# Kernel optimization log

Hardware: AMD Instinct MI355X
Metric: run time of the kernel (lower is better)

## Reference

```python
import jax, jax.numpy as jnp
import numpy as np

BATCH, N_MACS_PREV, CMS_PREV, NEUR_PREV = 256, 512, 8, 16
FILTER_LEN = 256
NUM_CMS, NUM_NEURONS = 32, 32
NUM_INPUTS = FILTER_LEN * CMS_PREV * NEUR_PREV  # 32768


def setup_inputs() -> dict:
    key = jax.random.key(0)
    k1, k2, k3 = jax.random.split(key, 3)
    x = jax.random.uniform(k1, (BATCH, N_MACS_PREV, CMS_PREV, NEUR_PREV), dtype=jnp.float32)
    input_filter = jax.random.randint(k2, (FILTER_LEN,), 0, N_MACS_PREV)
    # binary {0,1} weights, matching torch.randint(0, 2, ..., dtype=float32)
    weights = jax.random.randint(k3, (NUM_CMS, NUM_INPUTS, NUM_NEURONS), 0, 2).astype(jnp.float32)
    return {"x": x, "input_filter": input_filter, "weights": weights}


def reference(x, input_filter, weights):
    B = x.shape[0]
    # gather receptive field MACs and flatten: (B, num_inputs)
    xg = jnp.take(x, input_filter, axis=1).reshape(B, -1)
    # sum-normalize, nan_to_num handles all-zero rows (0/0 -> 0)
    xn = jnp.nan_to_num(xg / jnp.sum(xg, axis=-1, keepdims=True))
    # batched matmul: (B,I) x (C,I,N) -> (B,C,N)  (torch does (C,B,N) then permutes)
    acts = jnp.einsum('bi,cin->bcn', xn, weights)
    # familiarity-based softmax temperature
    familiarities = jnp.max(acts, axis=-1)          # (B, C)
    avg_fam = jnp.mean(familiarities)               # scalar
    softmax_temp = 1.0 / (avg_fam + 1e-4) - 1.0
    logits = acts / softmax_temp
    # categorical sample per (batch, cm); fixed key for determinism
    samples = jax.random.categorical(jax.random.key(42), logits, axis=-1)  # (B, C)
    # scatter one-hot write-out, int output as in torch
    out = jax.nn.one_hot(samples, NUM_NEURONS, dtype=jnp.int32)  # (B, C, N)
    return out
```

## Files before the change

kernel.cpp:

```cpp
#include <hip/hip_runtime.h>
#include <stdint.h>

#define BATCH 256
#define NMAC  512
#define ROWF  128
#define I_    32768
#define C_    32
#define N_    32
#define XROW  (NMAC * ROWF)
#define NCH   64

typedef float  f32x4  __attribute__((ext_vector_type(4)));
typedef __bf16 bf16x8 __attribute__((ext_vector_type(8)));

__device__ __forceinline__ uint32_t f2bf_rne(float f) {
    uint32_t u = __builtin_bit_cast(uint32_t, f);
    return (u + 0x7FFFu + ((u >> 16) & 1u)) >> 16;
}

__global__ __launch_bounds__(256) void k_sum(const float* __restrict__ x,
                                             const int* __restrict__ filt,
                                             float* __restrict__ S) {
    const int b = blockIdx.x;
    const int t = threadIdx.x;
    const float* xb = x + (size_t)b * XROW;
    float s = 0.f;
    for (int it = 0; it < 32; ++it) {
        int idx4 = it * 256 + t;
        int f = idx4 >> 5;
        int j4 = idx4 & 31;
        float4 v = *(const float4*)(xb + (size_t)filt[f] * ROWF + j4 * 4);
        s += v.x + v.y + v.z + v.w;
    }
    for (int o = 32; o > 0; o >>= 1) s += __shfl_down(s, o, 64);
    __shared__ float red[4];
    if ((t & 63) == 0) red[t >> 6] = s;
    __syncthreads();
    if (t == 0) S[b] = red[0] + red[1] + red[2] + red[3];
}

__global__ __launch_bounds__(256, 2) void k_gemm(const float* __restrict__ x,
                                                 const int* __restrict__ filt,
                                                 const float* __restrict__ w,
                                                 float* __restrict__ part,
                                                 float* __restrict__ raw,
                                                 int use_part) {
    __shared__ __align__(16) unsigned short afr[32 * 512];
    __shared__ __align__(16) unsigned short wfr[8 * 512];

    const int t  = threadIdx.x;
    const int l  = t & 63;
    const int wv = t >> 6;
    const int chunk = blockIdx.x & 63;
    const int c0 = (blockIdx.x >> 6) * 4;

    f32x4 acc[4][8];
#pragma unroll
    for (int bt = 0; bt < 4; ++bt)
#pragma unroll
        for (int ct = 0; ct < 8; ++ct) acc[bt][ct] = f32x4{0.f, 0.f, 0.f, 0.f};

    const int ar     = t >> 3;
    const int ai     = t & 7;
    const int a_quad = ai >> 1;
    const int a_j    = (ai & 1) * 4;
    const int wn = t & 31;
    const int wc = t >> 5;

    for (int st = 0; st < 16; ++st) {
        const int ifull = chunk * 512 + st * 32;
        const int fidx  = filt[ifull >> 7];
        const int ioff  = ifull & 127;
        const float* xs = x + (size_t)fidx * ROWF + ioff;

#pragma unroll
        for (int rr = 0; rr < 8; ++rr) {
            int row = rr * 32 + ar;
            float4 v = *(const float4*)(xs + (size_t)row * XROW + ai * 4);
            uint32_t u0 = __builtin_bit_cast(uint32_t, v.x);
            uint32_t u1 = __builtin_bit_cast(uint32_t, v.y);
            uint32_t u2 = __builtin_bit_cast(uint32_t, v.z);
            uint32_t u3 = __builtin_bit_cast(uint32_t, v.w);
            float l0 = v.x - __builtin_bit_cast(float, u0 & 0xFFFF0000u);
            float l1 = v.y - __builtin_bit_cast(float, u1 & 0xFFFF0000u);
            float l2 = v.z - __builtin_bit_cast(float, u2 & 0xFFFF0000u);
            float l3 = v.w - __builtin_bit_cast(float, u3 & 0xFFFF0000u);
            uint2 hp, lp;
            hp.x = (u0 >> 16) | (u1 & 0xFFFF0000u);
            hp.y = (u2 >> 16) | (u3 & 0xFFFF0000u);
            lp.x = f2bf_rne(l0) | (f2bf_rne(l1) << 16);
            lp.y = f2bf_rne(l2) | (f2bf_rne(l3) << 16);
            int rt   = row >> 4;
            int lane = a_quad * 16 + (row & 15);
            int base = (rt * 2) * 512 + lane * 8 + a_j;
            *(uint2*)&afr[base]       = hp;
            *(uint2*)&afr[base + 512] = lp;
        }

#pragma unroll
        for (int q = 0; q < 8; ++q) {
            int sl  = wc + 8 * q;
            int c   = sl >> 4;
            int il  = (sl & 15) * 2;
            const float* wp = w + ((size_t)(c0 + c) * I_ + ifull + il) * N_ + wn;
            uint32_t u0 = __builtin_bit_cast(uint32_t, wp[0]);
            uint32_t u1 = __builtin_bit_cast(uint32_t, wp[N_]);
            uint32_t pk = (u0 >> 16) | (u1 & 0xFFFF0000u);
            int lane = (il >> 3) * 16 + (wn & 15);
            int ct   = c * 2 + (wn >> 4);
            *(uint32_t*)&wfr[ct * 512 + lane * 8 + (il & 7)] = pk;
        }
        __syncthreads();

        bf16x8 av[4][2];
#pragma unroll
        for (int bt = 0; bt < 4; ++bt)
#pragma unroll
            for (int p = 0; p < 2; ++p)
                av[bt][p] = *(const bf16x8*)&afr[((wv * 4 + bt) * 2 + p) * 512 + l * 8];
        bf16x8 bv[8];
#pragma unroll
        for (int ct = 0; ct < 8; ++ct)
            bv[ct] = *(const bf16x8*)&wfr[ct * 512 + l * 8];
#pragma unroll
        for (int bt = 0; bt < 4; ++bt)
#pragma unroll
            for (int ct = 0; ct < 8; ++ct) {
                acc[bt][ct] = __builtin_amdgcn_mfma_f32_16x16x32_bf16(av[bt][0], bv[ct], acc[bt][ct], 0, 0, 0);
                acc[bt][ct] = __builtin_amdgcn_mfma_f32_16x16x32_bf16(av[bt][1], bv[ct], acc[bt][ct], 0, 0, 0);
            }
        __syncthreads();
    }

    const int quad = l >> 4, n15 = l & 15;
    if (use_part) {
        float* dst = part + (size_t)chunk * (BATCH * C_ * N_);
#pragma unroll
        for (int bt = 0; bt < 4; ++bt) {
#pragma unroll
            for (int ct = 0; ct < 8; ++ct) {
                int c = c0 + (ct >> 1);
                int n = (ct & 1) * 16 + n15;
#pragma unroll
                for (int r = 0; r < 4; ++r) {
                    int b = (wv * 4 + bt) * 16 + quad * 4 + r;
                    dst[((size_t)b * C_ + c) * N_ + n] = acc[bt][ct][r];
                }
            }
        }
    } else {
#pragma unroll
        for (int bt = 0; bt < 4; ++bt) {
#pragma unroll
            for (int ct = 0; ct < 8; ++ct) {
                int c = c0 + (ct >> 1);
                int n = (ct & 1) * 16 + n15;
#pragma unroll
                for (int r = 0; r < 4; ++r) {
                    int b = (wv * 4 + bt) * 16 + quad * 4 + r;
                    atomicAdd(&raw[((size_t)b * C_ + c) * N_ + n], acc[bt][ct][r]);
                }
            }
        }
    }
}

__global__ __launch_bounds__(256) void k_reduce(const float* __restrict__ part,
                                                const float* __restrict__ S,
                                                float* __restrict__ raw,
                                                float* __restrict__ fam) {
    const int i4 = blockIdx.x * 256 + threadIdx.x;
    const f32x4* p = (const f32x4*)part;
    f32x4 s = f32x4{0.f, 0.f, 0.f, 0.f};
#pragma unroll 8
    for (int ch = 0; ch < NCH; ++ch) s += p[(size_t)ch * 65536 + i4];
    ((f32x4*)raw)[i4] = s;
    float m = fmaxf(fmaxf(s[0], s[1]), fmaxf(s[2], s[3]));
    m = fmaxf(m, __shfl_xor(m, 1, 64));
    m = fmaxf(m, __shfl_xor(m, 2, 64));
    m = fmaxf(m, __shfl_xor(m, 4, 64));
    int r = i4 >> 3;
    float v = ((i4 & 7) == 0) ? (m / S[r >> 5]) : 0.f;
    for (int o = 32; o > 0; o >>= 1) v += __shfl_down(v, o, 64);
    __shared__ float red[4];
    if ((threadIdx.x & 63) == 0) red[threadIdx.x >> 6] = v;
    __syncthreads();
    if (threadIdx.x == 0) atomicAdd(fam, red[0] + red[1] + red[2] + red[3]);
}

__global__ __launch_bounds__(256) void k_fam(const float* __restrict__ raw,
                                             const float* __restrict__ S,
                                             float* __restrict__ fam) {
    int r = blockIdx.x * 256 + threadIdx.x;
    const float4* ap = (const float4*)(raw + (size_t)r * N_);
    float m = -3.0e38f;
#pragma unroll
    for (int q = 0; q < 8; ++q) {
        float4 v = ap[q];
        m = fmaxf(m, fmaxf(fmaxf(v.x, v.y), fmaxf(v.z, v.w)));
    }
    m = m / S[r >> 5];
    for (int o = 32; o > 0; o >>= 1) m += __shfl_down(m, o, 64);
    __shared__ float red[4];
    if ((threadIdx.x & 63) == 0) red[threadIdx.x >> 6] = m;
    __syncthreads();
    if (threadIdx.x == 0) atomicAdd(fam, red[0] + red[1] + red[2] + red[3]);
}

__device__ __forceinline__ uint32_t rotl32(uint32_t x, uint32_t r) {
    return (x << r) | (x >> (32u - r));
}
__device__ __forceinline__ void threefry(uint32_t k0, uint32_t k1,
                                         uint32_t x0, uint32_t x1,
                                         uint32_t& o0, uint32_t& o1) {
    uint32_t ks2 = k0 ^ k1 ^ 0x1BD11BDAu;
    x0 += k0; x1 += k1;
    x0 += x1; x1 = rotl32(x1, 13); x1 ^= x0;
    x0 += x1; x1 = rotl32(x1, 15); x1 ^= x0;
    x0 += x1; x1 = rotl32(x1, 26); x1 ^= x0;
    x0 += x1; x1 = rotl32(x1, 6);  x1 ^= x0;
    x0 += k1; x1 += ks2 + 1u;
    x0 += x1; x1 = rotl32(x1, 17); x1 ^= x0;
    x0 += x1; x1 = rotl32(x1, 29); x1 ^= x0;
    x0 += x1; x1 = rotl32(x1, 16); x1 ^= x0;
    x0 += x1; x1 = rotl32(x1, 24); x1 ^= x0;
    x0 += ks2; x1 += k0 + 2u;
    x0 += x1; x1 = rotl32(x1, 13); x1 ^= x0;
    x0 += x1; x1 = rotl32(x1, 15); x1 ^= x0;
    x0 += x1; x1 = rotl32(x1, 26); x1 ^= x0;
    x0 += x1; x1 = rotl32(x1, 6);  x1 ^= x0;
    x0 += k0; x1 += k1 + 3u;
    x0 += x1; x1 = rotl32(x1, 17); x1 ^= x0;
    x0 += x1; x1 = rotl32(x1, 29); x1 ^= x0;
    x0 += x1; x1 = rotl32(x1, 16); x1 ^= x0;
    x0 += x1; x1 = rotl32(x1, 24); x1 ^= x0;
    x0 += k1; x1 += ks2 + 4u;
    x0 += x1; x1 = rotl32(x1, 13); x1 ^= x0;
    x0 += x1; x1 = rotl32(x1, 15); x1 ^= x0;
    x0 += x1; x1 = rotl32(x1, 26); x1 ^= x0;
    x0 += x1; x1 = rotl32(x1, 6);  x1 ^= x0;
    x0 += ks2; x1 += k0 + 5u;
    o0 = x0; o1 = x1;
}

__device__ __forceinline__ float gumbel_of(uint32_t bits) {
    uint32_t fb = (bits >> 9) | 0x3F800000u;
    float f = __builtin_bit_cast(float, fb) - 1.0f;
    float u = f + 1.17549435e-38f;
    return -logf(-logf(u));
}

__global__ __launch_bounds__(256) void k_sample(const float* __restrict__ raw,
                                                const float* __restrict__ S,
                                                const float* __restrict__ fam,
                                                int* __restrict__ out) {
    int r0 = blockIdx.x * 256 + threadIdx.x;
    int r1 = r0 + 4096;
    float avg  = fam[0] * (1.0f / 8192.0f);
    float temp = 1.0f / (avg + 1e-4f) - 1.0f;
    float sA = S[r0 >> 5], sB = S[r1 >> 5];
    const float* apA = raw + (size_t)r0 * N_;
    const float* apB = raw + (size_t)r1 * N_;

    float bestA = -3.4e38f, bestB = -3.4e38f;
    int biA = 0, biB = 0;
    for (int n = 0; n < 32; ++n) {
        uint32_t iA = (uint32_t)(r0 * 32 + n);
        uint32_t iB = (uint32_t)(r1 * 32 + n);
        uint32_t a0, a1, b0, b1;
        threefry(0u, 42u, 0u, iA, a0, a1);
        threefry(0u, 42u, 0u, iB, b0, b1);
        float vA = (apA[n] / sA) / temp + gumbel_of(a0 ^ a1);
        float vB = (apB[n] / sB) / temp + gumbel_of(b0 ^ b1);
        if (vA > bestA) { bestA = vA; biA = n; }
        if (vB > bestB) { bestB = vB; biB = n; }
    }
    int4* opA = (int4*)(out + (size_t)r0 * N_);
    int4* opB = (int4*)(out + (size_t)r1 * N_);
#pragma unroll
    for (int q = 0; q < 8; ++q) {
        int4 a, b;
        a.x = (q * 4 + 0) == biA; a.y = (q * 4 + 1) == biA;
        a.z = (q * 4 + 2) == biA; a.w = (q * 4 + 3) == biA;
        b.x = (q * 4 + 0) == biB; b.y = (q * 4 + 1) == biB;
        b.z = (q * 4 + 2) == biB; b.w = (q * 4 + 3) == biB;
        opA[q] = a; opB[q] = b;
    }
}

extern "C" void kernel_launch(void* const* d_in, const int* in_sizes, int n_in,
                              void* d_out, int out_size, void* d_ws, size_t ws_size,
                              hipStream_t stream) {
    const float* x    = (const float*)d_in[0];
    const int*   filt = (const int*)d_in[1];
    const float* w    = (const float*)d_in[2];
    int* out = (int*)d_out;

    char* ws = (char*)d_ws;
    float* raw  = (float*)ws;
    float* fam  = (float*)(ws + (1 << 20));
    float* S    = (float*)(ws + (1 << 20) + 128);
    float* part = (float*)(ws + (2u << 20));

    const size_t need = (2u << 20) + (size_t)NCH * (BATCH * C_ * N_) * sizeof(float);
    const int use_part = (ws_size >= need) ? 1 : 0;

    if (use_part) {
        hipMemsetAsync(ws + (1 << 20), 0, 128, stream);
        hipLaunchKernelGGL(k_sum,    dim3(256), dim3(256), 0, stream, x, filt, S);
        hipLaunchKernelGGL(k_gemm,   dim3(512), dim3(256), 0, stream, x, filt, w, part, raw, 1);
        hipLaunchKernelGGL(k_reduce, dim3(256), dim3(256), 0, stream, part, S, raw, fam);
        hipLaunchKernelGGL(k_sample, dim3(16),  dim3(256), 0, stream, raw, S, fam, out);
    } else {
        hipMemsetAsync(ws, 0, (1 << 20) + 128, stream);
        hipLaunchKernelGGL(k_sum,    dim3(256), dim3(256), 0, stream, x, filt, S);
        hipLaunchKernelGGL(k_gemm,   dim3(512), dim3(256), 0, stream, x, filt, w, part, raw, 0);
        hipLaunchKernelGGL(k_fam,    dim3(32),  dim3(256), 0, stream, raw, S, fam);
        hipLaunchKernelGGL(k_sample, dim3(16),  dim3(256), 0, stream, raw, S, fam, out);
    }
}
```

Measured before the change: 280.7 us.

## Pre-split activations into bf16 fragments and double-buffer GEMM loads via LDS DMA

Adds a prep kernel that gathers the filtered activations once, splits them into hi/lo bf16 pairs and writes them in MFMA fragment layout to workspace. The new GEMM kernel double-buffers A tiles with global_load_lds DMA and prefetches weights into registers for the next stage, overlapping loads with MFMA work. This removes the per-block repeated gather and conversion of x across the 8 c-groups, but it adds a 32 MB intermediate write and read and needs a larger workspace. The old path is kept as a fallback.

```diff
diff --git a/kernel.cpp b/kernel.cpp
--- a/kernel.cpp
+++ b/kernel.cpp
@@ -9,6 +9,7 @@
 #define N_    32
 #define XROW  (NMAC * ROWF)
 #define NCH   64
+#define NST   16
 
 typedef float  f32x4  __attribute__((ext_vector_type(4)));
 typedef __bf16 bf16x8 __attribute__((ext_vector_type(8)));
@@ -16,6 +17,12 @@
 __device__ __forceinline__ uint32_t f2bf_rne(float f) {
     uint32_t u = __builtin_bit_cast(uint32_t, f);
     return (u + 0x7FFFu + ((u >> 16) & 1u)) >> 16;
+}
+
+__device__ __forceinline__ void gll16(const void* g, void* l) {
+    __builtin_amdgcn_global_load_lds(
+        (const __attribute__((address_space(1))) uint32_t*)g,
+        (__attribute__((address_space(3))) uint32_t*)l, 16, 0, 0);
 }
 
 __global__ __launch_bounds__(256) void k_sum(const float* __restrict__ x,
@@ -39,12 +46,150 @@
     if (t == 0) S[b] = red[0] + red[1] + red[2] + red[3];
 }
 
-__global__ __launch_bounds__(256, 2) void k_gemm(const float* __restrict__ x,
-                                                 const int* __restrict__ filt,
-                                                 const float* __restrict__ w,
-                                                 float* __restrict__ part,
-                                                 float* __restrict__ raw,
-                                                 int use_part) {
+__global__ __launch_bounds__(256) void k_prep(const float* __restrict__ x,
+                                              const int* __restrict__ filt,
+                                              unsigned short* __restrict__ prepA) {
+    const int b     = threadIdx.x;
+    const int chunk = blockIdx.x >> 4;
+    const int st    = blockIdx.x & 15;
+    const int ifull = chunk * 512 + st * 32;
+    const int fidx  = filt[ifull >> 7];
+    const int ioff  = ifull & 127;
+    const float* src = x + (size_t)b * XROW + (size_t)fidx * ROWF + ioff;
+    unsigned short* dstb = prepA + (size_t)blockIdx.x * 16384
+                         + (b >> 4) * 1024 + (b & 15) * 8;
+    float4 v[8];
+#pragma unroll
+    for (int j = 0; j < 8; ++j) v[j] = ((const float4*)src)[j];
+#pragma unroll
+    for (int kq = 0; kq < 4; ++kq) {
+        float f[8];
+        float4 a = v[kq * 2], c = v[kq * 2 + 1];
+        f[0] = a.x; f[1] = a.y; f[2] = a.z; f[3] = a.w;
+        f[4] = c.x; f[5] = c.y; f[6] = c.z; f[7] = c.w;
+        uint32_t h[4], lo[4];
+#pragma unroll
+        for (int e = 0; e < 4; ++e) {
+            uint32_t u0 = __builtin_bit_cast(uint32_t, f[2 * e]);
+            uint32_t u1 = __builtin_bit_cast(uint32_t, f[2 * e + 1]);
+            float r0 = f[2 * e]     - __builtin_bit_cast(float, u0 & 0xFFFF0000u);
+            float r1 = f[2 * e + 1] - __builtin_bit_cast(float, u1 & 0xFFFF0000u);
+            h[e]  = (u0 >> 16) | (u1 & 0xFFFF0000u);
+            lo[e] = f2bf_rne(r0) | (f2bf_rne(r1) << 16);
+        }
+        *(uint4*)&dstb[kq * 128]       = make_uint4(h[0], h[1], h[2], h[3]);
+        *(uint4*)&dstb[512 + kq * 128] = make_uint4(lo[0], lo[1], lo[2], lo[3]);
+    }
+}
+
+__global__ __launch_bounds__(256, 2) void k_gemm2(const unsigned short* __restrict__ prepA,
+                                                  const float* __restrict__ w,
+                                                  float* __restrict__ part) {
+    __shared__ __align__(16) unsigned short bufA[2][16384];
+    __shared__ __align__(16) unsigned short bufW[2][4096];
+
+    const int t  = threadIdx.x;
+    const int l  = t & 63;
+    const int wv = t >> 6;
+    const int chunk = blockIdx.x & 63;
+    const int c0 = (blockIdx.x >> 6) * 4;
+
+    const char* Abase = (const char*)(prepA + (size_t)chunk * NST * 16384);
+    const int wn = t & 31;
+    const int wc = t >> 5;
+
+    f32x4 acc[4][8];
+#pragma unroll
+    for (int bt = 0; bt < 4; ++bt)
+#pragma unroll
+        for (int ct = 0; ct < 8; ++ct) acc[bt][ct] = f32x4{0.f, 0.f, 0.f, 0.f};
+
+    uint32_t Wr[8];
+
+    auto issueA = [&](int st, int bsel) {
+        const char* s = Abase + (size_t)st * 32768 + wv * 1024 + l * 16;
+        char* d = ((char*)&bufA[bsel][0]) + wv * 1024;
+#pragma unroll
+        for (int r = 0; r < 8; ++r)
+            gll16(s + r * 4096, d + r * 4096);
+    };
+    auto loadW = [&](int st) {
+        const int ifull = chunk * 512 + st * 32;
+#pragma unroll
+        for (int q = 0; q < 8; ++q) {
+            int sl = wc + 8 * q;
+            int c  = sl >> 4;
+            int il = (sl & 15) * 2;
+            const float* wp = w + ((size_t)(c0 + c) * I_ + ifull + il) * N_ + wn;
+            uint32_t u0 = __builtin_bit_cast(uint32_t, wp[0]);
+            uint32_t u1 = __builtin_bit_cast(uint32_t, wp[N_]);
+            Wr[q] = (u0 >> 16) | (u1 & 0xFFFF0000u);
+        }
+    };
+    auto storeW = [&](int bsel) {
+#pragma unroll
+        for (int q = 0; q < 8; ++q) {
+            int sl = wc + 8 * q;
+            int c  = sl >> 4;
+            int il = (sl & 15) * 2;
+            int lane = (il >> 3) * 16 + (wn & 15);
+            int ct   = c * 2 + (wn >> 4);
+            *(uint32_t*)&bufW[bsel][ct * 512 + lane * 8 + (il & 7)] = Wr[q];
+        }
+    };
+
+    issueA(0, 0);
+    loadW(0); storeW(0);
+    __syncthreads();
+
+    for (int st = 0; st < NST; ++st) {
+        const int cur = st & 1, nxt = cur ^ 1;
+        if (st + 1 < NST) { issueA(st + 1, nxt); loadW(st + 1); }
+
+        bf16x8 av[4][2];
+#pragma unroll
+        for (int bt = 0; bt < 4; ++bt)
+#pragma unroll
+            for (int p = 0; p < 2; ++p)
+                av[bt][p] = *(const bf16x8*)&bufA[cur][((wv * 4 + bt) * 2 + p) * 512 + l * 8];
+        bf16x8 bv[8];
+#pragma unroll
+        for (int ct = 0; ct < 8; ++ct)
+            bv[ct] = *(const bf16x8*)&bufW[cur][ct * 512 + l * 8];
+#pragma unroll
+        for (int bt = 0; bt < 4; ++bt)
+#pragma unroll
+            for (int ct = 0; ct < 8; ++ct) {
+                acc[bt][ct] = __builtin_amdgcn_mfma_f32_16x16x32_bf16(av[bt][0], bv[ct], acc[bt][ct], 0, 0, 0);
+                acc[bt][ct] = __builtin_amdgcn_mfma_f32_16x16x32_bf16(av[bt][1], bv[ct], acc[bt][ct], 0, 0, 0);
+            }
+        if (st + 1 < NST) storeW(nxt);
+        __syncthreads();
+    }
+
+    const int quad = l >> 4, n15 = l & 15;
+    float* dst = part + (size_t)chunk * (BATCH * C_ * N_);
+#pragma unroll
+    for (int bt = 0; bt < 4; ++bt) {
+#pragma unroll
+        for (int ct = 0; ct < 8; ++ct) {
+            int c = c0 + (ct >> 1);
+            int n = (ct & 1) * 16 + n15;
+#pragma unroll
+            for (int r = 0; r < 4; ++r) {
+                int b = (wv * 4 + bt) * 16 + quad * 4 + r;
+                dst[((size_t)b * C_ + c) * N_ + n] = acc[bt][ct][r];
+            }
+        }
+    }
+}
+
+__global__ __launch_bounds__(256, 2) void k_gemm_fb(const float* __restrict__ x,
+                                                    const int* __restrict__ filt,
+                                                    const float* __restrict__ w,
+                                                    float* __restrict__ part,
+                                                    float* __restrict__ raw,
+                                                    int use_part) {
     __shared__ __align__(16) unsigned short afr[32 * 512];
     __shared__ __align__(16) unsigned short wfr[8 * 512];
 
@@ -96,7 +241,6 @@
             *(uint2*)&afr[base]       = hp;
             *(uint2*)&afr[base + 512] = lp;
         }
-
 #pragma unroll
         for (int q = 0; q < 8; ++q) {
             int sl  = wc + 8 * q;
@@ -136,7 +280,7 @@
     if (use_part) {
         float* dst = part + (size_t)chunk * (BATCH * C_ * N_);
 #pragma unroll
-        for (int bt = 0; bt < 4; ++bt) {
+        for (int bt = 0; bt < 4; ++bt)
 #pragma unroll
             for (int ct = 0; ct < 8; ++ct) {
                 int c = c0 + (ct >> 1);
@@ -147,10 +291,9 @@
                     dst[((size_t)b * C_ + c) * N_ + n] = acc[bt][ct][r];
                 }
             }
-        }
     } else {
 #pragma unroll
-        for (int bt = 0; bt < 4; ++bt) {
+        for (int bt = 0; bt < 4; ++bt)
 #pragma unroll
             for (int ct = 0; ct < 8; ++ct) {
                 int c = c0 + (ct >> 1);
@@ -161,7 +304,6 @@
                     atomicAdd(&raw[((size_t)b * C_ + c) * N_ + n], acc[bt][ct][r]);
                 }
             }
-        }
     }
 }
 
@@ -301,20 +443,28 @@
     float* fam  = (float*)(ws + (1 << 20));
     float* S    = (float*)(ws + (1 << 20) + 128);
     float* part = (float*)(ws + (2u << 20));
-
-    const size_t need = (2u << 20) + (size_t)NCH * (BATCH * C_ * N_) * sizeof(float);
-    const int use_part = (ws_size >= need) ? 1 : 0;
-
-    if (use_part) {
+    unsigned short* prepA = (unsigned short*)(ws + (66u << 20));
+
+    const size_t need_part = (2u << 20) + (size_t)NCH * (BATCH * C_ * N_) * sizeof(float);
+    const size_t need_prep = need_part + (size_t)NCH * NST * 16384 * sizeof(unsigned short);
+
+    if (ws_size >= need_prep) {
+        hipMemsetAsync(ws + (1 << 20), 0, 128, stream);
+        hipLaunchKernelGGL(k_prep,   dim3(1024), dim3(256), 0, stream, x, filt, prepA);
+        hipLaunchKernelGGL(k_sum,    dim3(256),  dim3(256), 0, stream, x, filt, S);
+        hipLaunchKernelGGL(k_gemm2,  dim3(512),  dim3(256), 0, stream, prepA, w, part);
+        hipLaunchKernelGGL(k_reduce, dim3(256),  dim3(256), 0, stream, part, S, raw, fam);
+        hipLaunchKernelGGL(k_sample, dim3(16),   dim3(256), 0, stream, raw, S, fam, out);
+    } else if (ws_size >= need_part) {
         hipMemsetAsync(ws + (1 << 20), 0, 128, stream);
         hipLaunchKernelGGL(k_sum,    dim3(256), dim3(256), 0, stream, x, filt, S);
-        hipLaunchKernelGGL(k_gemm,   dim3(512), dim3(256), 0, stream, x, filt, w, part, raw, 1);
+        hipLaunchKernelGGL(k_gemm_fb, dim3(512), dim3(256), 0, stream, x, filt, w, part, raw, 1);
         hipLaunchKernelGGL(k_reduce, dim3(256), dim3(256), 0, stream, part, S, raw, fam);
         hipLaunchKernelGGL(k_sample, dim3(16),  dim3(256), 0, stream, raw, S, fam, out);
     } else {
         hipMemsetAsync(ws, 0, (1 << 20) + 128, stream);
         hipLaunchKernelGGL(k_sum,    dim3(256), dim3(256), 0, stream, x, filt, S);
-        hipLaunchKernelGGL(k_gemm,   dim3(512), dim3(256), 0, stream, x, filt, w, part, raw, 0);
+        hipLaunchKernelGGL(k_gemm_fb, dim3(512), dim3(256), 0, stream, x, filt, w, part, raw, 0);
         hipLaunchKernelGGL(k_fam,    dim3(32),  dim3(256), 0, stream, raw, S, fam);
         hipLaunchKernelGGL(k_sample, dim3(16),  dim3(256), 0, stream, raw, S, fam, out);
     }
```

Result: slower. 297.5 us (+6.0%).
